# Performance work log

Measured on AMD Instinct MI355X. Metric: run time of the kernel, lower is better.

## Reference

```python
import jax, jax.numpy as jnp
import numpy as np

B, L, D, C = 4, 512, 128, 128
EPS = 1e-7  # Keras backend epsilon


def setup_inputs() -> dict:
    key = jax.random.key(0)
    ks = jax.random.split(key, 4)
    inps = jax.random.normal(ks[0], (B, L, D), dtype=jnp.float32)
    # glorot_normal-ish scale for weights
    wei_t = jax.random.normal(ks[1], (D, C), dtype=jnp.float32) * (2.0 / (D + C)) ** 0.5
    wei_x = jax.random.normal(ks[2], (D, C), dtype=jnp.float32) * (2.0 / (D + C)) ** 0.5
    bxh = jnp.zeros((C,), dtype=jnp.float32)
    wei_a = jax.random.normal(ks[3], (C,), dtype=jnp.float32) * (2.0 / (C + 1)) ** 0.5
    bxa = jnp.zeros((), dtype=jnp.float32)
    return {"inps": inps, "wei_t": wei_t, "wei_x": wei_x, "bxh": bxh,
            "wei_a": wei_a, "bxa": bxa}


def reference(inps, wei_t, wei_x, bxh, wei_a, bxa):
    # Additive (Bahdanau-style) pairwise self-attention, no mask.
    qt = inps @ wei_t                      # [B, L, C] (query-side projection)
    kx = inps @ wei_x                      # [B, L, C] (key-side projection)
    # Pairwise hidden: [B, L, L, C]
    h = jnp.tanh(qt[:, :, None, :] + kx[:, None, :, :] + bxh)
    scores = jnp.einsum('bijc,c->bij', h, wei_a) + bxa  # [B, L, L]
    # activation_func=None -> linear (identity)
    e = jnp.exp(scores - jnp.max(scores, axis=-1, keepdims=True))
    a = e / (jnp.sum(e, axis=-1, keepdims=True) + EPS)   # [B, L, L]
    out = jnp.einsum('bij,bjd->bid', a, inps)            # [B, L, D]
    return out
```

## Files before the change

### kernel.cpp

```cpp
#include <hip/hip_runtime.h>

#define NB 4
#define SL 512
#define DD 128
#define CC 128

__device__ __forceinline__ float fexp2(float x) { return __builtin_amdgcn_exp2f(x); }
__device__ __forceinline__ float frcp(float x)  { return __builtin_amdgcn_rcpf(x); }

__global__ __launch_bounds__(256) void proj_kernel(
    const float* __restrict__ inps, const float* __restrict__ wei_t,
    const float* __restrict__ wei_x, const float* __restrict__ bxh,
    float* __restrict__ E, float* __restrict__ F)
{
    const float K2 = 2.8853900817779268f;
    const int row0 = blockIdx.x * 2;
    const int b    = row0 >> 9;
    const int i0   = row0 & 511;
    const int c    = threadIdx.x & 127;
    const int sel  = threadIdx.x >> 7;

    const float* W  = sel ? wei_x : wei_t;
    const float* r0 = inps + (size_t)row0 * DD;
    const float* r1 = r0 + DD;

    float a0 = 0.f, a1 = 0.f;
    #pragma unroll 8
    for (int k = 0; k < DD; ++k) {
        float w = W[k * CC + c];
        a0 = fmaf(r0[k], w, a0);
        a1 = fmaf(r1[k], w, a1);
    }

    if (sel == 0) {
        float bb = bxh[c];
        E[(size_t)(row0 + 0) * CC + c] = fexp2(K2 * (a0 + bb));
        E[(size_t)(row0 + 1) * CC + c] = fexp2(K2 * (a1 + bb));
    } else {
        float2 v = {fexp2(K2 * a0), fexp2(K2 * a1)};
        *reinterpret_cast<float2*>(&F[((size_t)b * CC + c) * SL + i0]) = v;
    }
}

__global__ __launch_bounds__(512, 4) void attn_kernel(
    const float* __restrict__ inps, const float* __restrict__ wei_a,
    const float* __restrict__ E, const float* __restrict__ F,
    float* __restrict__ out)
{
    __shared__ float4 upk[CC];
    __shared__ float pool[4 * 16 * DD];
    __shared__ float scT[SL * 4];
    __shared__ float redw[4 * 4];

    const int blk = blockIdx.x;
    const int b   = blk >> 7;
    const int i0  = (blk & 127) * 4;
    const int bi0 = b * SL + i0;
    const int tid = threadIdx.x;
    const int jt  = tid & 255;
    const int ch  = tid >> 8;
    const int j0  = jt * 2;

    if (tid < CC) {
        float4 u;
        u.x = E[(size_t)(bi0 + 0) * CC + tid];
        u.y = E[(size_t)(bi0 + 1) * CC + tid];
        u.z = E[(size_t)(bi0 + 2) * CC + tid];
        u.w = E[(size_t)(bi0 + 3) * CC + tid];
        upk[tid] = u;
    }
    __syncthreads();

    const int c0 = ch * 64;
    const float* fb = F + ((size_t)b * CC + c0) * SL + j0;
    const float4* up = upk + c0;
    const float* wa = wei_a + c0;
    float sx[4] = {0.f, 0.f, 0.f, 0.f};
    float sy[4] = {0.f, 0.f, 0.f, 0.f};
    #pragma unroll 4
    for (int cp = 0; cp < 32; ++cp) {
        float2 f0 = *reinterpret_cast<const float2*>(&fb[(size_t)(2 * cp) * SL]);
        float2 f1 = *reinterpret_cast<const float2*>(&fb[(size_t)(2 * cp + 1) * SL]);
        float4 u0 = up[2 * cp];
        float4 u1 = up[2 * cp + 1];
        float wa0 = wa[2 * cp], wa1 = wa[2 * cp + 1];
        const float* u0p = reinterpret_cast<const float*>(&u0);
        const float* u1p = reinterpret_cast<const float*>(&u1);
        #pragma unroll
        for (int i = 0; i < 4; ++i) {
            float ax = fmaf(u0p[i], f0.x, 1.0f);
            float bx = fmaf(u1p[i], f1.x, 1.0f);
            float numx = fmaf(wa0, bx, wa1 * ax);
            sx[i] = fmaf(numx, frcp(ax * bx), sx[i]);
            float ay = fmaf(u0p[i], f0.y, 1.0f);
            float by = fmaf(u1p[i], f1.y, 1.0f);
            float numy = fmaf(wa0, by, wa1 * ay);
            sy[i] = fmaf(numy, frcp(ay * by), sy[i]);
        }
    }

    if (ch == 1) {
        float* m = &pool[jt * 9];
        #pragma unroll
        for (int i = 0; i < 4; ++i) { m[i] = sx[i]; m[4 + i] = sy[i]; }
    }
    __syncthreads();

    if (ch == 0) {
        {
            const float* m = &pool[jt * 9];
            #pragma unroll
            for (int i = 0; i < 4; ++i) { sx[i] += m[i]; sy[i] += m[4 + i]; }
        }
        const float KE = -2.8853900817779268f;
        float ex[4], ey[4];
        const int lane = tid & 63, wv = tid >> 6;
        #pragma unroll
        for (int i = 0; i < 4; ++i) {
            ex[i] = fexp2(sx[i] * KE);
            ey[i] = fexp2(sy[i] * KE);
            float t = ex[i] + ey[i];
            #pragma unroll
            for (int off = 32; off > 0; off >>= 1)
                t += __shfl_xor(t, off, 64);
            if (lane == 0) redw[i * 4 + wv] = t;
        }
        __syncthreads();
        float4 av0, av1;
        {
            float S0 = redw[0] + redw[1] + redw[2] + redw[3];
            float S1 = redw[4] + redw[5] + redw[6] + redw[7];
            float S2 = redw[8] + redw[9] + redw[10] + redw[11];
            float S3 = redw[12] + redw[13] + redw[14] + redw[15];
            float r0 = frcp(S0 + 1e-7f), r1 = frcp(S1 + 1e-7f);
            float r2 = frcp(S2 + 1e-7f), r3 = frcp(S3 + 1e-7f);
            av0 = make_float4(ex[0] * r0, ex[1] * r1, ex[2] * r2, ex[3] * r3);
            av1 = make_float4(ey[0] * r0, ey[1] * r1, ey[2] * r2, ey[3] * r3);
        }
        *reinterpret_cast<float4*>(&scT[j0 * 4])     = av0;
        *reinterpret_cast<float4*>(&scT[j0 * 4 + 4]) = av1;
    } else {
        __syncthreads();
    }
    __syncthreads();

    {
        const int dq = (tid & 31) * 4;
        const int jq = tid >> 5;
        const float* ibase = inps + (size_t)b * SL * DD;
        float4 acc0 = {0,0,0,0}, acc1 = {0,0,0,0}, acc2 = {0,0,0,0}, acc3 = {0,0,0,0};
        const int jb = jq * 32;
        #pragma unroll 4
        for (int jj = 0; jj < 32; ++jj) {
            int jx = jb + jj;
            float4 v  = *reinterpret_cast<const float4*>(ibase + (size_t)jx * DD + dq);
            float4 a4 = *reinterpret_cast<const float4*>(&scT[jx * 4]);
            acc0.x = fmaf(a4.x, v.x, acc0.x); acc0.y = fmaf(a4.x, v.y, acc0.y);
            acc0.z = fmaf(a4.x, v.z, acc0.z); acc0.w = fmaf(a4.x, v.w, acc0.w);
            acc1.x = fmaf(a4.y, v.x, acc1.x); acc1.y = fmaf(a4.y, v.y, acc1.y);
            acc1.z = fmaf(a4.y, v.z, acc1.z); acc1.w = fmaf(a4.y, v.w, acc1.w);
            acc2.x = fmaf(a4.z, v.x, acc2.x); acc2.y = fmaf(a4.z, v.y, acc2.y);
            acc2.z = fmaf(a4.z, v.z, acc2.z); acc2.w = fmaf(a4.z, v.w, acc2.w);
            acc3.x = fmaf(a4.w, v.x, acc3.x); acc3.y = fmaf(a4.w, v.y, acc3.y);
            acc3.z = fmaf(a4.w, v.z, acc3.z); acc3.w = fmaf(a4.w, v.w, acc3.w);
        }
        *reinterpret_cast<float4*>(&pool[(0 * 16 + jq) * DD + dq]) = acc0;
        *reinterpret_cast<float4*>(&pool[(1 * 16 + jq) * DD + dq]) = acc1;
        *reinterpret_cast<float4*>(&pool[(2 * 16 + jq) * DD + dq]) = acc2;
        *reinterpret_cast<float4*>(&pool[(3 * 16 + jq) * DD + dq]) = acc3;
    }
    __syncthreads();

    {
        int i = tid >> 7, d = tid & 127;
        float sum = 0.f;
        #pragma unroll
        for (int q = 0; q < 16; ++q) sum += pool[(i * 16 + q) * DD + d];
        out[(size_t)(bi0 + i) * DD + d] = sum;
    }
}

extern "C" void kernel_launch(void* const* d_in, const int* in_sizes, int n_in,
                              void* d_out, int out_size, void* d_ws, size_t ws_size,
                              hipStream_t stream) {
    const float* inps  = (const float*)d_in[0];
    const float* wei_t = (const float*)d_in[1];
    const float* wei_x = (const float*)d_in[2];
    const float* bxh   = (const float*)d_in[3];
    const float* wei_a = (const float*)d_in[4];
    float* out = (float*)d_out;

    float* E = (float*)d_ws;
    float* F = E + (size_t)NB * SL * CC;

    proj_kernel<<<NB * SL / 2, 256, 0, stream>>>(inps, wei_t, wei_x, bxh, E, F);
    attn_kernel<<<NB * SL / 4, 512, 0, stream>>>(inps, wei_a, E, F, out);
}
```

Baseline: 90.86 us.

## Fuse query projection into attention kernel and retile score loop 4x4

The query-side projection and its exp transform move into the attention kernel, so the E buffer and its global round trip go away. The projection kernel now computes only F. The pairwise score loop is retiled so each thread handles 4 query rows by 4 key columns over a quarter of the channels, using float4 loads of F to reuse each loaded value across more FMAs. The softmax reduction is redistributed across all 512 threads with a padded shared buffer. The cost is extra per-block projection work before the main loop and higher register pressure from the 16 accumulators.

```diff
diff --git a/kernel.cpp b/kernel.cpp
--- a/kernel.cpp
+++ b/kernel.cpp
@@ -8,139 +8,123 @@
 __device__ __forceinline__ float fexp2(float x) { return __builtin_amdgcn_exp2f(x); }
 __device__ __forceinline__ float frcp(float x)  { return __builtin_amdgcn_rcpf(x); }
 
-__global__ __launch_bounds__(256) void proj_kernel(
-    const float* __restrict__ inps, const float* __restrict__ wei_t,
-    const float* __restrict__ wei_x, const float* __restrict__ bxh,
-    float* __restrict__ E, float* __restrict__ F)
+__global__ __launch_bounds__(256) void projF_kernel(
+    const float* __restrict__ inps, const float* __restrict__ wei_x,
+    float* __restrict__ F)
 {
     const float K2 = 2.8853900817779268f;
-    const int row0 = blockIdx.x * 2;
+    const int row0 = blockIdx.x * 4;
     const int b    = row0 >> 9;
-    const int i0   = row0 & 511;
+    const int l0   = row0 & 511;
     const int c    = threadIdx.x & 127;
-    const int sel  = threadIdx.x >> 7;
+    const int h    = threadIdx.x >> 7;
 
-    const float* W  = sel ? wei_x : wei_t;
-    const float* r0 = inps + (size_t)row0 * DD;
+    const float* r0 = inps + (size_t)(row0 + 2 * h) * DD;
     const float* r1 = r0 + DD;
 
     float a0 = 0.f, a1 = 0.f;
     #pragma unroll 8
     for (int k = 0; k < DD; ++k) {
-        float w = W[k * CC + c];
+        float w = wei_x[k * CC + c];
         a0 = fmaf(r0[k], w, a0);
         a1 = fmaf(r1[k], w, a1);
     }
-
-    if (sel == 0) {
-        float bb = bxh[c];
-        E[(size_t)(row0 + 0) * CC + c] = fexp2(K2 * (a0 + bb));
-        E[(size_t)(row0 + 1) * CC + c] = fexp2(K2 * (a1 + bb));
-    } else {
-        float2 v = {fexp2(K2 * a0), fexp2(K2 * a1)};
-        *reinterpret_cast<float2*>(&F[((size_t)b * CC + c) * SL + i0]) = v;
-    }
+    float2 v = {fexp2(K2 * a0), fexp2(K2 * a1)};
+    *reinterpret_cast<float2*>(&F[((size_t)b * CC + c) * SL + l0 + 2 * h]) = v;
 }
 
 __global__ __launch_bounds__(512, 4) void attn_kernel(
-    const float* __restrict__ inps, const float* __restrict__ wei_a,
-    const float* __restrict__ E, const float* __restrict__ F,
-    float* __restrict__ out)
+    const float* __restrict__ inps, const float* __restrict__ wei_t,
+    const float* __restrict__ bxh,  const float* __restrict__ wei_a,
+    const float* __restrict__ F,    float* __restrict__ out)
 {
     __shared__ float4 upk[CC];
-    __shared__ float pool[4 * 16 * DD];
+    __shared__ float pool[4 * 128 * 17];
     __shared__ float scT[SL * 4];
-    __shared__ float redw[4 * 4];
+    __shared__ float redw[4 * 2];
 
+    const float K2 = 2.8853900817779268f;
     const int blk = blockIdx.x;
     const int b   = blk >> 7;
     const int i0  = (blk & 127) * 4;
     const int bi0 = b * SL + i0;
     const int tid = threadIdx.x;
-    const int jt  = tid & 255;
-    const int ch  = tid >> 8;
-    const int j0  = jt * 2;
 
-    if (tid < CC) {
-        float4 u;
-        u.x = E[(size_t)(bi0 + 0) * CC + tid];
-        u.y = E[(size_t)(bi0 + 1) * CC + tid];
-        u.z = E[(size_t)(bi0 + 2) * CC + tid];
-        u.w = E[(size_t)(bi0 + 3) * CC + tid];
-        upk[tid] = u;
+    {
+        const int r = tid >> 7;
+        const int c = tid & 127;
+        const float* rp = inps + (size_t)(bi0 + r) * DD;
+        float acc = 0.f;
+        #pragma unroll 8
+        for (int k = 0; k < DD; ++k)
+            acc = fmaf(rp[k], wei_t[k * CC + c], acc);
+        ((float*)&upk[c])[r] = fexp2(K2 * (acc + bxh[c]));
     }
     __syncthreads();
 
-    const int c0 = ch * 64;
+    const int jg = tid & 127;
+    const int cq = tid >> 7;
+    const int j0 = jg * 4;
+    const int c0 = cq * 32;
     const float* fb = F + ((size_t)b * CC + c0) * SL + j0;
     const float4* up = upk + c0;
     const float* wa = wei_a + c0;
-    float sx[4] = {0.f, 0.f, 0.f, 0.f};
-    float sy[4] = {0.f, 0.f, 0.f, 0.f};
-    #pragma unroll 4
-    for (int cp = 0; cp < 32; ++cp) {
-        float2 f0 = *reinterpret_cast<const float2*>(&fb[(size_t)(2 * cp) * SL]);
-        float2 f1 = *reinterpret_cast<const float2*>(&fb[(size_t)(2 * cp + 1) * SL]);
+    float ac[4][4] = {{0.f,0.f,0.f,0.f},{0.f,0.f,0.f,0.f},
+                      {0.f,0.f,0.f,0.f},{0.f,0.f,0.f,0.f}};
+    #pragma unroll 2
+    for (int cp = 0; cp < 16; ++cp) {
+        float4 f0 = *reinterpret_cast<const float4*>(&fb[(size_t)(2 * cp) * SL]);
+        float4 f1 = *reinterpret_cast<const float4*>(&fb[(size_t)(2 * cp + 1) * SL]);
         float4 u0 = up[2 * cp];
         float4 u1 = up[2 * cp + 1];
         float wa0 = wa[2 * cp], wa1 = wa[2 * cp + 1];
         const float* u0p = reinterpret_cast<const float*>(&u0);
         const float* u1p = reinterpret_cast<const float*>(&u1);
+        const float* f0p = reinterpret_cast<const float*>(&f0);
+        const float* f1p = reinterpret_cast<const float*>(&f1);
         #pragma unroll
         for (int i = 0; i < 4; ++i) {
-            float ax = fmaf(u0p[i], f0.x, 1.0f);
-            float bx = fmaf(u1p[i], f1.x, 1.0f);
-            float numx = fmaf(wa0, bx, wa1 * ax);
-            sx[i] = fmaf(numx, frcp(ax * bx), sx[i]);
-            float ay = fmaf(u0p[i], f0.y, 1.0f);
-            float by = fmaf(u1p[i], f1.y, 1.0f);
-            float numy = fmaf(wa0, by, wa1 * ay);
-            sy[i] = fmaf(numy, frcp(ay * by), sy[i]);
+            #pragma unroll
+            for (int j = 0; j < 4; ++j) {
+                float ax = fmaf(u0p[i], f0p[j], 1.0f);
+                float bx = fmaf(u1p[i], f1p[j], 1.0f);
+                float num = fmaf(wa0, bx, wa1 * ax);
+                ac[i][j] = fmaf(num, frcp(ax * bx), ac[i][j]);
+            }
         }
     }
-
-    if (ch == 1) {
-        float* m = &pool[jt * 9];
+    {
+        float* m = &pool[cq * 2176 + jg * 17];
         #pragma unroll
-        for (int i = 0; i < 4; ++i) { m[i] = sx[i]; m[4 + i] = sy[i]; }
+        for (int i = 0; i < 4; ++i)
+            #pragma unroll
+            for (int j = 0; j < 4; ++j)
+                m[i * 4 + j] = ac[i][j];
     }
     __syncthreads();
 
-    if (ch == 0) {
-        {
-            const float* m = &pool[jt * 9];
-            #pragma unroll
-            for (int i = 0; i < 4; ++i) { sx[i] += m[i]; sy[i] += m[4 + i]; }
+    {
+        float s0 = 0.f, s1 = 0.f, s2 = 0.f, s3 = 0.f;
+        #pragma unroll
+        for (int seg = 0; seg < 4; ++seg) {
+            const float* m = &pool[seg * 2176 + jg * 17 + cq * 4];
+            s0 += m[0]; s1 += m[1]; s2 += m[2]; s3 += m[3];
         }
         const float KE = -2.8853900817779268f;
-        float ex[4], ey[4];
-        const int lane = tid & 63, wv = tid >> 6;
+        float e0 = fexp2(s0 * KE), e1 = fexp2(s1 * KE);
+        float e2 = fexp2(s2 * KE), e3 = fexp2(s3 * KE);
+        float p = (e0 + e1) + (e2 + e3);
         #pragma unroll
-        for (int i = 0; i < 4; ++i) {
-            ex[i] = fexp2(sx[i] * KE);
-            ey[i] = fexp2(sy[i] * KE);
-            float t = ex[i] + ey[i];
-            #pragma unroll
-            for (int off = 32; off > 0; off >>= 1)
-                t += __shfl_xor(t, off, 64);
-            if (lane == 0) redw[i * 4 + wv] = t;
-        }
+        for (int off = 32; off > 0; off >>= 1)
+            p += __shfl_xor(p, off, 64);
+        if ((tid & 63) == 0) redw[cq * 2 + ((tid >> 6) & 1)] = p;
         __syncthreads();
-        float4 av0, av1;
-        {
-            float S0 = redw[0] + redw[1] + redw[2] + redw[3];
-            float S1 = redw[4] + redw[5] + redw[6] + redw[7];
-            float S2 = redw[8] + redw[9] + redw[10] + redw[11];
-            float S3 = redw[12] + redw[13] + redw[14] + redw[15];
-            float r0 = frcp(S0 + 1e-7f), r1 = frcp(S1 + 1e-7f);
-            float r2 = frcp(S2 + 1e-7f), r3 = frcp(S3 + 1e-7f);
-            av0 = make_float4(ex[0] * r0, ex[1] * r1, ex[2] * r2, ex[3] * r3);
-            av1 = make_float4(ey[0] * r0, ey[1] * r1, ey[2] * r2, ey[3] * r3);
-        }
-        *reinterpret_cast<float4*>(&scT[j0 * 4])     = av0;
-        *reinterpret_cast<float4*>(&scT[j0 * 4 + 4]) = av1;
-    } else {
-        __syncthreads();
+        float S  = redw[cq * 2] + redw[cq * 2 + 1];
+        float rS = frcp(S + 1e-7f);
+        scT[(j0    ) * 4 + cq] = e0 * rS;
+        scT[(j0 + 1) * 4 + cq] = e1 * rS;
+        scT[(j0 + 2) * 4 + cq] = e2 * rS;
+        scT[(j0 + 3) * 4 + cq] = e3 * rS;
     }
     __syncthreads();
 
@@ -190,9 +174,8 @@
     const float* wei_a = (const float*)d_in[4];
     float* out = (float*)d_out;
 
-    float* E = (float*)d_ws;
-    float* F = E + (size_t)NB * SL * CC;
+    float* F = (float*)d_ws;
 
-    proj_kernel<<<NB * SL / 2, 256, 0, stream>>>(inps, wei_t, wei_x, bxh, E, F);
-    attn_kernel<<<NB * SL / 4, 512, 0, stream>>>(inps, wei_a, E, F, out);
+    projF_kernel<<<NB * SL / 4, 256, 0, stream>>>(inps, wei_x, F);
+    attn_kernel<<<NB * SL / 4, 512, 0, stream>>>(inps, wei_t, bxh, wei_a, F, out);
 }
```

New measurement: 95.57 us. 1.05x slower.
